# Performance work log

Measured on AMD Instinct MI355X. Metric: run time of the kernel, lower is better.

Reference implementation:

```python
import jax, jax.numpy as jnp
import numpy as np

B, N, D, H, DEPTH = 2, 2048, 768, 12, 4
DH = D // H
SCALE = DH ** -0.5
EPS = 1e-5
FF = 4 * D


def layer_norm(x, w, b):
    m = jnp.mean(x, axis=-1, keepdims=True)
    v = jnp.mean((x - m) ** 2, axis=-1, keepdims=True)
    return (x - m) * jax.lax.rsqrt(v + EPS) * w + b


def to_heads(t):  # [b, n, D] -> [b, H, n, DH]
    b, n, _ = t.shape
    return t.reshape(b, n, H, DH).transpose(0, 2, 1, 3)


def merge_heads(t):  # [b, H, n, DH] -> [b, n, D]
    b, h, n, dh = t.shape
    return t.transpose(0, 2, 1, 3).reshape(b, n, D)


def attend(q, k, v, bias):
    s = jnp.einsum('bhid,bhjd->bhij', q, k) * SCALE + bias
    a = jax.nn.softmax(s, axis=-1)
    return merge_heads(jnp.einsum('bhij,bhjd->bhid', a, v))


def setup_inputs():
    key = jax.random.key(0)
    ks = iter(jax.random.split(key, 16))

    def p(shape, scale=0.02):
        return jax.random.normal(next(ks), shape, dtype=jnp.float32) * scale

    inp = {
        'x': jax.random.normal(next(ks), (B, N, D), dtype=jnp.float32),
        'context': jax.random.normal(next(ks), (B, N, D), dtype=jnp.float32),
        'relative_position_bias': jax.random.normal(next(ks), (1, H, N, N), dtype=jnp.float32) * 0.02,
        # self-attn params (stacked over depth)
        'ln1_w': jnp.ones((DEPTH, D), jnp.float32), 'ln1_b': jnp.zeros((DEPTH, D), jnp.float32),
        'w_qkv': p((DEPTH, D, 3 * D)),
        'w_so': p((DEPTH, D, D)), 'b_so': jnp.zeros((DEPTH, D), jnp.float32),
        # cross-attn params (shared LN applied to x and context, as in source)
        'ln2_w': jnp.ones((DEPTH, D), jnp.float32), 'ln2_b': jnp.zeros((DEPTH, D), jnp.float32),
        'w_q': p((DEPTH, D, D)), 'w_k': p((DEPTH, D, D)), 'w_v': p((DEPTH, D, D)),
        'w_co': p((DEPTH, D, D)), 'b_co': jnp.zeros((DEPTH, D), jnp.float32),
        # FFN params
        'ln3_w': jnp.ones((DEPTH, D), jnp.float32), 'ln3_b': jnp.zeros((DEPTH, D), jnp.float32),
        'w_f1': p((DEPTH, D, FF)), 'b_f1': jnp.zeros((DEPTH, FF), jnp.float32),
        'w_f2': p((DEPTH, FF, D)), 'b_f2': jnp.zeros((DEPTH, D), jnp.float32),
        # final norm
        'lnout_w': jnp.ones((D,), jnp.float32), 'lnout_b': jnp.zeros((D,), jnp.float32),
    }
    return inp


def reference(x, context, relative_position_bias,
              ln1_w, ln1_b, w_qkv, w_so, b_so,
              ln2_w, ln2_b, w_q, w_k, w_v, w_co, b_co,
              ln3_w, ln3_b, w_f1, b_f1, w_f2, b_f2,
              lnout_w, lnout_b):
    bias = relative_position_bias
    for i in range(DEPTH):
        # self-attention block (pre-norm, residual)
        xn = layer_norm(x, ln1_w[i], ln1_b[i])
        q, k, v = jnp.split(xn @ w_qkv[i], 3, axis=-1)
        o = attend(to_heads(q), to_heads(k), to_heads(v), bias)
        x = o @ w_so[i] + b_so[i] + x
        # cross-attention block (input_norm shared for x and context)
        xn = layer_norm(x, ln2_w[i], ln2_b[i])
        cn = layer_norm(context, ln2_w[i], ln2_b[i])
        o = attend(to_heads(xn @ w_q[i]), to_heads(cn @ w_k[i]), to_heads(cn @ w_v[i]), bias)
        x = o @ w_co[i] + b_co[i] + x
        # FFN block
        xn = layer_norm(x, ln3_w[i], ln3_b[i])
        h = jax.nn.gelu(xn @ w_f1[i] + b_f1[i], approximate=False)
        x = h @ w_f2[i] + b_f2[i] + x
    return layer_norm(x, lnout_w, lnout_b)
```

## Files before the change

kernel.cpp:

```cpp
#include <hip/hip_runtime.h>
#include <cstdint>
#include <cstddef>

#define DEV static __device__ __forceinline__

typedef float  f32x4 __attribute__((ext_vector_type(4)));
typedef float  f32x2 __attribute__((ext_vector_type(2)));
typedef short  s16x8 __attribute__((ext_vector_type(8)));
typedef unsigned short u16;
typedef unsigned int   u32;
typedef unsigned int   u32x4 __attribute__((ext_vector_type(4)));
typedef unsigned short u16x2 __attribute__((ext_vector_type(2)));
typedef unsigned short u16x4 __attribute__((ext_vector_type(4)));
typedef __bf16 bf16x8 __attribute__((ext_vector_type(8)));

#define LOG2E 1.4426950408889634f
#define QSCALE_CONST 0.18033688011112042f
#define BSCALE 256.0f
#define BINV   0.00390625f

DEV u16 f2bf(float f){ return __builtin_bit_cast(u16, (__bf16)f); }
DEV float bf2f(u16 v){ union { unsigned u; float f; } x; x.u = ((unsigned)v) << 16; return x.f; }

DEV float fexp2(float x){
#if __has_builtin(__builtin_amdgcn_exp2f)
  return __builtin_amdgcn_exp2f(x);
#else
  return exp2f(x);
#endif
}

DEV f32x4 mfma16(s16x8 a, s16x8 b, f32x4 c){
  return __builtin_amdgcn_mfma_f32_16x16x32_bf16(
      __builtin_bit_cast(bf16x8, a), __builtin_bit_cast(bf16x8, b), c, 0, 0, 0);
}

DEV void gld16(const void* g, void* l){
  __builtin_amdgcn_global_load_lds(
      (const __attribute__((address_space(1))) void*)(uintptr_t)g,
      (__attribute__((address_space(3))) void*)(unsigned)(uintptr_t)l,
      16, 0, 0);
}

#if __has_builtin(__builtin_amdgcn_cvt_pk_fp8_f32) && __has_builtin(__builtin_amdgcn_cvt_pk_f32_fp8)
DEV u32 pk4_fp8(f32x4 v){
  int r = __builtin_amdgcn_cvt_pk_fp8_f32(v[0], v[1], 0, false);
  r     = __builtin_amdgcn_cvt_pk_fp8_f32(v[2], v[3], r, true);
  return (u32)r;
}
template<bool HI>
DEV f32x2 upk_fp8(u32 w){
  return __builtin_amdgcn_cvt_pk_f32_fp8((int)w, HI);
}
#else
DEV unsigned enc1(float x){
  union{float f; unsigned u;} c; c.f = x;
  unsigned s = (c.u >> 24) & 0x80;
  int e = (int)((c.u >> 23) & 0xff) - 127;
  unsigned m = c.u & 0x7fffff;
  if (e >= -6){
    unsigned mant = m >> 20, rem = m & 0xfffff;
    if (rem > 0x80000 || (rem == 0x80000 && (mant & 1))) mant++;
    unsigned eb = (unsigned)(e + 7);
    if (mant == 8){ mant = 0; eb++; }
    if (eb >= 16){ eb = 15; mant = 6; }
    return s | (eb << 3) | mant;
  }
  if (e < -10) return s;
  int sh = -6 - e;
  unsigned full = (1u << 23) | m;
  unsigned mant = full >> (20 + sh);
  unsigned rem  = full & ((1u << (20 + sh)) - 1);
  unsigned half = 1u << (19 + sh);
  if (rem > half || (rem == half && (mant & 1))) mant++;
  if (mant == 8) return s | (1u << 3);
  return s | mant;
}
DEV u32 pk4_fp8(f32x4 v){
  return enc1(v[0]) | (enc1(v[1]) << 8) | (enc1(v[2]) << 16) | (enc1(v[3]) << 24);
}
DEV float dec1(unsigned b){
  int s = (b >> 7) & 1, e = (b >> 3) & 15; float m = (float)(b & 7) * 0.125f;
  float v = e ? ldexpf(1.0f + m, e - 7) : ldexpf(m, -6);
  return s ? -v : v;
}
template<bool HI>
DEV f32x2 upk_fp8(u32 w){
  unsigned lo = HI ? ((w >> 16) & 0xff) : (w & 0xff);
  unsigned h2 = HI ? ((w >> 24) & 0xff) : ((w >> 8) & 0xff);
  f32x2 r; r[0] = dec1(lo); r[1] = dec1(h2); return r;
}
#endif

__global__ void __launch_bounds__(256)
transpose_cvt(const float* __restrict__ src, u16* __restrict__ dst, int K, int N,
              size_t dzstride){
  int z = blockIdx.z;
  src += (size_t)z * K * N;
  dst += (size_t)z * dzstride;
  __shared__ float t[32][33];
  int n0 = blockIdx.x * 32, k0 = blockIdx.y * 32;
#pragma unroll
  for (int i = 0; i < 4; ++i)
    t[threadIdx.y + 8*i][threadIdx.x] = src[(size_t)(k0 + threadIdx.y + 8*i) * N + n0 + threadIdx.x];
  __syncthreads();
#pragma unroll
  for (int i = 0; i < 4; ++i)
    dst[(size_t)(n0 + threadIdx.y + 8*i) * K + k0 + threadIdx.x] = f2bf(t[threadIdx.x][threadIdx.y + 8*i]);
}

struct TPtrs { const float* src[20]; u16* dst[20]; };
__global__ void __launch_bounds__(256)
transpose_cvt_batch(TPtrs tp){
  const float* src = tp.src[blockIdx.z];
  u16* dst = tp.dst[blockIdx.z];
  __shared__ float t[32][33];
  int n0 = blockIdx.x * 32, k0 = blockIdx.y * 32;
#pragma unroll
  for (int i = 0; i < 4; ++i)
    t[threadIdx.y + 8*i][threadIdx.x] = src[(size_t)(k0 + threadIdx.y + 8*i) * 768 + n0 + threadIdx.x];
  __syncthreads();
#pragma unroll
  for (int i = 0; i < 4; ++i)
    dst[(size_t)(n0 + threadIdx.y + 8*i) * 768 + k0 + threadIdx.x] = f2bf(t[threadIdx.x][threadIdx.y + 8*i]);
}

__global__ void __launch_bounds__(256)
cvt_biasT(const float* __restrict__ in, unsigned char* __restrict__ out){
  const int kvt = blockIdx.x, qt = blockIdx.y, h = blockIdx.z, tid = threadIdx.x;
  const int q  = qt * 64 + ((tid >> 6) << 4) + (tid & 15);
  const int c0 = kvt * 64 + ((tid >> 4) & 3) * 4;
  const float* src = in + ((size_t)h * 2048 + q) * 2048;
  u32x4 wv;
#pragma unroll
  for (int mi = 0; mi < 4; ++mi){
    f32x4 v = *(const f32x4*)(src + c0 + mi * 16);
#pragma unroll
    for (int r = 0; r < 4; ++r) v[r] = fminf(fmaxf(v[r] * (LOG2E * BSCALE), -448.f), 448.f);
    wv[mi] = pk4_fp8(v);
  }
  *(u32x4*)(out + ((size_t)(h * 32 + qt) * 32 + kvt) * 4096 + tid * 16) = wv;
}

__global__ void __launch_bounds__(256)
ln_pre(const float* __restrict__ x, const float* __restrict__ ctx,
       const float* __restrict__ w1, const float* __restrict__ b1,
       const float* __restrict__ w2, const float* __restrict__ b2,
       u16* __restrict__ xn, u16* __restrict__ xbuf, u16* __restrict__ cn){
  const int wv = threadIdx.x >> 6, lane = threadIdx.x & 63;
  const int row = blockIdx.x * 4 + wv;
  const float* xr = (blockIdx.y == 0 ? x : ctx) + (size_t)row * 768;
  f32x4 t[3]; float s = 0.f, s2 = 0.f;
#pragma unroll
  for (int c = 0; c < 3; ++c){
    t[c] = *(const f32x4*)(xr + c * 256 + lane * 4);
#pragma unroll
    for (int j = 0; j < 4; ++j){ s += t[c][j]; s2 += t[c][j] * t[c][j]; }
  }
#pragma unroll
  for (int off = 1; off < 64; off <<= 1){ s += __shfl_xor(s, off); s2 += __shfl_xor(s2, off); }
  float m = s * (1.f/768.f);
  float rstd = rsqrtf(s2 * (1.f/768.f) - m * m + 1e-5f);
  if (blockIdx.y == 0){
#pragma unroll
    for (int c = 0; c < 3; ++c){
      const int col = c * 256 + lane * 4;
      f32x4 wv4 = *(const f32x4*)(w1 + col);
      f32x4 bv4 = *(const f32x4*)(b1 + col);
      u16x4 o, xb;
#pragma unroll
      for (int j = 0; j < 4; ++j){
        o[j]  = f2bf((t[c][j] - m) * rstd * wv4[j] + bv4[j]);
        xb[j] = f2bf(t[c][j]);
      }
      *(u16x4*)(xn   + (size_t)row * 768 + col) = o;
      *(u16x4*)(xbuf + (size_t)row * 768 + col) = xb;
    }
  } else {
#pragma unroll
    for (int i = 0; i < 4; ++i){
      u16* dst = cn + (size_t)i * 4096 * 768 + (size_t)row * 768;
#pragma unroll
      for (int c = 0; c < 3; ++c){
        const int col = c * 256 + lane * 4;
        f32x4 wv4 = *(const f32x4*)(w2 + i * 768 + col);
        f32x4 bv4 = *(const f32x4*)(b2 + i * 768 + col);
        u16x4 o;
#pragma unroll
        for (int j = 0; j < 4; ++j) o[j] = f2bf((t[c][j] - m) * rstd * wv4[j] + bv4[j]);
        *(u16x4*)(dst + col) = o;
      }
    }
  }
}

template<typename OUT, int NZ>
__global__ void __launch_bounds__(256)
red_ln(const u16* __restrict__ pb, const float* __restrict__ biasrow,
       u16* __restrict__ xbuf, OUT* __restrict__ out,
       const float* __restrict__ lw, const float* __restrict__ lb){
  const int wv = threadIdx.x >> 6, lane = threadIdx.x & 63;
  const int row0 = blockIdx.x * 8 + wv * 2;
  const size_t S = 4096ll * 768;
  f32x4 t[2][3]; float s[2] = {0.f, 0.f}, s2[2] = {0.f, 0.f};
#pragma unroll
  for (int rr = 0; rr < 2; ++rr){
    const int row = row0 + rr;
    const u16* p0 = pb + (size_t)row * 768;
    u16* xr = xbuf + (size_t)row * 768;
#pragma unroll
    for (int c = 0; c < 3; ++c){
      const int col = c * 256 + lane * 4;
      f32x4 v = *(const f32x4*)(biasrow + col);
      u16x4 xv = *(const u16x4*)(xr + col);
#pragma unroll
      for (int j = 0; j < 4; ++j) v[j] += bf2f(xv[j]);
#pragma unroll
      for (int z = 0; z < NZ; ++z){
        u16x4 pv = *(const u16x4*)(p0 + z * S + col);
#pragma unroll
        for (int j = 0; j < 4; ++j) v[j] += bf2f(pv[j]);
      }
      u16x4 xo;
#pragma unroll
      for (int j = 0; j < 4; ++j) xo[j] = f2bf(v[j]);
      *(u16x4*)(xr + col) = xo;
      t[rr][c] = v;
#pragma unroll
      for (int j = 0; j < 4; ++j){ s[rr] += v[j]; s2[rr] += v[j] * v[j]; }
    }
  }
#pragma unroll
  for (int off = 1; off < 64; off <<= 1){
#pragma unroll
    for (int rr = 0; rr < 2; ++rr){
      s[rr]  += __shfl_xor(s[rr], off);
      s2[rr] += __shfl_xor(s2[rr], off);
    }
  }
#pragma unroll
  for (int rr = 0; rr < 2; ++rr){
    const int row = row0 + rr;
    float m = s[rr] * (1.f/768.f);
    float rstd = rsqrtf(s2[rr] * (1.f/768.f) - m * m + 1e-5f);
#pragma unroll
    for (int c = 0; c < 3; ++c){
      const int col = c * 256 + lane * 4;
      f32x4 wv4 = *(const f32x4*)(lw + col);
      f32x4 bv4 = *(const f32x4*)(lb + col);
      if constexpr (sizeof(OUT) == 2){
        u16x4 o;
#pragma unroll
        for (int j = 0; j < 4; ++j) o[j] = f2bf((t[rr][c][j] - m) * rstd * wv4[j] + bv4[j]);
        *(u16x4*)((u16*)out + (size_t)row * 768 + col) = o;
      } else {
        f32x4 o;
#pragma unroll
        for (int j = 0; j < 4; ++j) o[j] = (t[rr][c][j] - m) * rstd * wv4[j] + bv4[j];
        *(f32x4*)((float*)out + (size_t)row * 768 + col) = o;
      }
    }
  }
}

template<int EPI>
__global__ void __launch_bounds__(256)
gemm_bf16(const u16* __restrict__ A, int lda, const u16* __restrict__ Bt, int ldb,
          int nk, u16* __restrict__ Cb, int ldc,
          const float* __restrict__ bias,
          const u16* __restrict__ A2, const u16* __restrict__ Bt2){
  __shared__ u16 As[2][128 * 32];
  __shared__ u16 Bs[2][128 * 32];
  float colscale = 1.0f;
  if constexpr (EPI == 4){
    const int z = blockIdx.z;
    if (z == 0){ colscale = QSCALE_CONST; }
    else { A = A2; Bt = Bt2 + (size_t)(z - 1) * 768 * 768; }
    Cb += z * 768;
  }
  if constexpr (EPI == 5){
    const int z = blockIdx.z;
    A  += (size_t)z * nk * 32;
    Bt += (size_t)z * nk * 32;
    Cb += (size_t)z * 4096 * 768;
  }
  const int gx = gridDim.x, nwg = gx * gridDim.y;
  int lin = blockIdx.y * gx + blockIdx.x;
  {
    const int qq = nwg >> 3, rr = nwg & 7;
    const int xc = lin & 7, oo = lin >> 3;
    lin = (xc < rr ? xc * (qq + 1) : rr * (qq + 1) + (xc - rr) * qq) + oo;
  }
  const int m0 = (lin % gx) * 128, n0 = (lin / gx) * 128;

  const int tid = threadIdx.x, w = tid >> 6, lane = tid & 63;
  const int l16 = lane & 15, g = lane >> 4;
  const int wm = (w >> 1) * 64, wn = (w & 1) * 64;
  f32x4 acc[4][4] = {};

  const u16* a0 = A  + (size_t)(m0 + (tid >> 2)) * lda + (tid & 3) * 8;
  const u16* a1 = A  + (size_t)(m0 + (tid >> 2) + 64) * lda + (tid & 3) * 8;
  const u16* b0 = Bt + (size_t)(n0 + (tid >> 2)) * ldb + (tid & 3) * 8;
  const u16* b1 = Bt + (size_t)(n0 + (tid >> 2) + 64) * ldb + (tid & 3) * 8;

  {
    char* ab = (char*)As[0]; char* bb = (char*)Bs[0];
    gld16(a0, ab + w * 1024); gld16(a1, ab + 4096 + w * 1024);
    gld16(b0, bb + w * 1024); gld16(b1, bb + 4096 + w * 1024);
  }
  __syncthreads();

  int cb = 0;
  for (int kt = 0; kt < nk; ++kt){
    if (kt + 1 < nk){
      const int k1 = (kt + 1) * 32;
      char* ab = (char*)As[cb ^ 1]; char* bb = (char*)Bs[cb ^ 1];
      gld16(a0 + k1, ab + w * 1024); gld16(a1 + k1, ab + 4096 + w * 1024);
      gld16(b0 + k1, bb + w * 1024); gld16(b1 + k1, bb + 4096 + w * 1024);
    }
    const u16* Ab = As[cb]; const u16* Bb = Bs[cb];
    s16x8 af[4], bfv[4];
#pragma unroll
    for (int mi = 0; mi < 4; ++mi)
      af[mi] = *(const s16x8*)(Ab + (wm + mi*16 + l16) * 32 + 8 * g);
#pragma unroll
    for (int ni = 0; ni < 4; ++ni)
      bfv[ni] = *(const s16x8*)(Bb + (wn + ni*16 + l16) * 32 + 8 * g);
#pragma unroll
    for (int mi = 0; mi < 4; ++mi)
#pragma unroll
      for (int ni = 0; ni < 4; ++ni)
        acc[mi][ni] = mfma16(af[mi], bfv[ni], acc[mi][ni]);
    __syncthreads();
    cb ^= 1;
  }

#pragma unroll
  for (int mi = 0; mi < 4; ++mi){
    const int rg = m0 + wm + mi*16 + 4*g;
#pragma unroll
    for (int ni = 0; ni < 4; ++ni){
      const int col = n0 + wn + ni*16 + l16;
      f32x4 v = acc[mi][ni];
#pragma unroll
      for (int r = 0; r < 4; ++r){
        const int row = rg + r;
        if constexpr (EPI == 2){
          float t = v[r] + bias[col];
          float ge = 0.5f * t * (1.0f + erff(t * 0.7071067811865476f));
          Cb[(size_t)row * ldc + col] = f2bf(ge);
        } else if constexpr (EPI == 3){
          float sc = (col < 768) ? QSCALE_CONST : 1.0f;
          Cb[(size_t)row * ldc + col] = f2bf(v[r] * sc);
        } else if constexpr (EPI == 4){
          Cb[(size_t)row * ldc + col] = f2bf(v[r] * colscale);
        } else {
          Cb[(size_t)row * 768 + col] = f2bf(v[r]);
        }
      }
    }
  }
}

__global__ void __launch_bounds__(256)
attn_kernel(const u16* __restrict__ qkv, const unsigned char* __restrict__ biasT,
            u16* __restrict__ out){
  __shared__ __align__(16) u16 Ks[2][4096];
  __shared__ __align__(16) u16 Vt[2][4096];
  __shared__ __align__(16) u16 Pl[4][1024];

  const int tid = threadIdx.x, w = tid >> 6, lane = tid & 63;
  const int l16 = lane & 15, g = lane >> 4;
  const int qt = blockIdx.x, h = blockIdx.y, b = blockIdx.z;
  const int rowbase = b * 2048, q0 = qt * 64;

  const int ci0 = w * 64 + lane, ci1 = ci0 + 256;
  const int r0 = ci0 >> 3, sc0 = ci0 & 7, r1 = ci1 >> 3, sc1 = ci1 & 7;
  const u16* kp0 = qkv + (size_t)(rowbase + r0) * 2304 + 768 + h * 64 + (((sc0 ^ (r0 & 7)) & 7) << 3);
  const u16* kp1 = qkv + (size_t)(rowbase + r1) * 2304 + 768 + h * 64 + (((sc1 ^ (r1 & 7)) & 7) << 3);
  const int dh0 = (tid & 31) * 2, vs = tid >> 5;
  const u16* vp = qkv + (size_t)(rowbase + vs * 8) * 2304 + 1536 + h * 64 + dh0;
  u16x2 vr[8];
  const unsigned char* bT = biasT + ((size_t)(h * 32 + qt) * 32) * 4096 + tid * 16;
  u32x4 brW, bnW;

  const u16* qrow = qkv + (size_t)(rowbase + q0 + w * 16 + l16) * 2304 + h * 64;
  s16x8 qf0 = *(const s16x8*)(qrow + 8 * g);
  s16x8 qf1 = *(const s16x8*)(qrow + 32 + 8 * g);

  f32x4 oacc[4] = {};
  float mrun = -3.0e38f, lrun = 0.f;
  const int sw = l16 & 7;

  {
    char* kb = (char*)Ks[0] + w * 1024;
    gld16(kp0, kb); gld16(kp1, kb + 4096);
#pragma unroll
    for (int i = 0; i < 8; ++i) vr[i] = *(const u16x2*)(vp + (size_t)i * 2304);
    brW = *(const u32x4*)(bT);
    s16x8 vA, vB;
#pragma unroll
    for (int j = 0; j < 8; ++j){ vA[j] = (short)vr[j][0]; vB[j] = (short)vr[j][1]; }
    *(s16x8*)(Vt[0] + dh0 * 64 + ((vs ^ (dh0 & 7)) << 3)) = vA;
    *(s16x8*)(Vt[0] + (dh0 + 1) * 64 + ((vs ^ ((dh0 + 1) & 7)) << 3)) = vB;
  }
  __syncthreads();

  for (int t = 0; t < 32; ++t){
    const int cb = t & 1;
    if (t < 31){
      const size_t koff = (size_t)(t + 1) * 64 * 2304;
      char* kb = (char*)Ks[cb ^ 1] + w * 1024;
      gld16(kp0 + koff, kb); gld16(kp1 + koff, kb + 4096);
      const u16* p = vp + koff;
#pragma unroll
      for (int i = 0; i < 8; ++i) vr[i] = *(const u16x2*)(p + (size_t)i * 2304);
      bnW = *(const u32x4*)(bT + (size_t)(t + 1) * 4096);
    }

    f32x4 st[4];
    __builtin_amdgcn_s_setprio(1);
#pragma unroll
    for (int mi = 0; mi < 4; ++mi){
      const int row = l16 + 16 * mi;
      s16x8 kf0 = *(const s16x8*)(Ks[cb] + row * 64 + ((g ^ sw) << 3));
      s16x8 kf1 = *(const s16x8*)(Ks[cb] + row * 64 + (((g + 4) ^ sw) << 3));
      f32x4 z = {};
      z = mfma16(kf0, qf0, z);
      st[mi] = mfma16(kf1, qf1, z);
    }
    __builtin_amdgcn_s_setprio(0);

    float mloc[4];
#pragma unroll
    for (int mi = 0; mi < 4; ++mi){
      f32x2 lo = upk_fp8<false>(brW[mi]);
      f32x2 hi = upk_fp8<true>(brW[mi]);
      st[mi][0] = fmaf(lo[0], BINV, st[mi][0]);
      st[mi][1] = fmaf(lo[1], BINV, st[mi][1]);
      st[mi][2] = fmaf(hi[0], BINV, st[mi][2]);
      st[mi][3] = fmaf(hi[1], BINV, st[mi][3]);
      mloc[mi] = fmaxf(fmaxf(st[mi][0], st[mi][1]), fmaxf(st[mi][2], st[mi][3]));
    }
    float tmax = fmaxf(fmaxf(mloc[0], mloc[1]), fmaxf(mloc[2], mloc[3]));
    tmax = fmaxf(tmax, __shfl_xor(tmax, 16));
    tmax = fmaxf(tmax, __shfl_xor(tmax, 32));
    if (!__all(tmax <= mrun + 8.f)){
      float mnew = fmaxf(mrun, tmax);
      float al = fexp2(mrun - mnew);
      mrun = mnew;
      lrun *= al;
#pragma unroll
      for (int r = 0; r < 4; ++r){
        float aq = __shfl(al, 4 * g + r);
#pragma unroll
        for (int ni = 0; ni < 4; ++ni) oacc[ni][r] *= aq;
      }
    }
    float ssum = 0.f;
#pragma unroll
    for (int mi = 0; mi < 4; ++mi){
      u16x4 pk;
#pragma unroll
      for (int r = 0; r < 4; ++r){
        float pv = fexp2(st[mi][r] - mrun);
        ssum += pv;
        pk[r] = f2bf(pv);
      }
      *(u16x4*)(Pl[w] + l16 * 64 + (((2*mi + (g >> 1)) ^ sw) << 3) + 4 * (g & 1)) = pk;
    }
    ssum += __shfl_xor(ssum, 16);
    ssum += __shfl_xor(ssum, 32);
    lrun += ssum;

    __builtin_amdgcn_s_setprio(1);
#pragma unroll
    for (int ks2 = 0; ks2 < 2; ++ks2){
      s16x8 pf = *(const s16x8*)(Pl[w] + l16 * 64 + (((4*ks2 + g) ^ sw) << 3));
#pragma unroll
      for (int ni = 0; ni < 4; ++ni){
        const int dh = l16 + 16 * ni;
        s16x8 vf = *(const s16x8*)(Vt[cb] + dh * 64 + (((4*ks2 + g) ^ sw) << 3));
        oacc[ni] = mfma16(pf, vf, oacc[ni]);
      }
    }
    __builtin_amdgcn_s_setprio(0);

    if (t < 31){
      s16x8 vA, vB;
#pragma unroll
      for (int j = 0; j < 8; ++j){ vA[j] = (short)vr[j][0]; vB[j] = (short)vr[j][1]; }
      *(s16x8*)(Vt[cb ^ 1] + dh0 * 64 + ((vs ^ (dh0 & 7)) << 3)) = vA;
      *(s16x8*)(Vt[cb ^ 1] + (dh0 + 1) * 64 + ((vs ^ ((dh0 + 1) & 7)) << 3)) = vB;
      brW = bnW;
    }
    __syncthreads();
  }

#pragma unroll
  for (int r = 0; r < 4; ++r){
    float lq = __shfl(lrun, 4 * g + r);
    float inv = 1.0f / lq;
    const int row = rowbase + q0 + w * 16 + 4 * g + r;
#pragma unroll
    for (int ni = 0; ni < 4; ++ni)
      out[(size_t)row * 768 + h * 64 + l16 + 16 * ni] = f2bf(oacc[ni][r] * inv);
  }
}

extern "C" void kernel_launch(void* const* d_in, const int* in_sizes, int n_in,
                              void* d_out, int out_size, void* d_ws, size_t ws_size,
                              hipStream_t stream){
  const float* in_x    = (const float*)d_in[0];
  const float* in_ctx  = (const float*)d_in[1];
  const float* in_bias = (const float*)d_in[2];
  const float* ln1_w = (const float*)d_in[3];
  const float* ln1_b = (const float*)d_in[4];
  const float* w_qkv = (const float*)d_in[5];
  const float* w_so  = (const float*)d_in[6];
  const float* b_so  = (const float*)d_in[7];
  const float* ln2_w = (const float*)d_in[8];
  const float* ln2_b = (const float*)d_in[9];
  const float* w_q   = (const float*)d_in[10];
  const float* w_k   = (const float*)d_in[11];
  const float* w_v   = (const float*)d_in[12];
  const float* w_co  = (const float*)d_in[13];
  const float* b_co  = (const float*)d_in[14];
  const float* ln3_w = (const float*)d_in[15];
  const float* ln3_b = (const float*)d_in[16];
  const float* w_f1  = (const float*)d_in[17];
  const float* b_f1  = (const float*)d_in[18];
  const float* w_f2  = (const float*)d_in[19];
  const float* b_f2  = (const float*)d_in[20];
  const float* lnout_w = (const float*)d_in[21];
  const float* lnout_b = (const float*)d_in[22];

  char* p = (char*)d_ws;
  u16* xbuf    = (u16*)p;    p += 4096ll * 768 * 2;
  u16* pbuf    = (u16*)p;    p += 4ll * 4096 * 768 * 2;
  u16* xn      = (u16*)p;    p += 4096ll * 768 * 2;
  u16* cn      = (u16*)p;    p += 4ll * 4096 * 768 * 2;
  u16* qkvb    = (u16*)p;    p += 4096ll * 2304 * 2;
  u16* attO    = (u16*)p;    p += 4096ll * 768 * 2;
  u16* ffh     = (u16*)p;    p += 4096ll * 3072 * 2;
  u16* wqkvT   = (u16*)p;    p += 4ll * 2304 * 768 * 2;
  u16* wsoT    = (u16*)p;    p += 4ll * 768 * 768 * 2;
  u16* wqT     = (u16*)p;    p += 4ll * 768 * 768 * 2;
  u16* wkvT    = (u16*)p;    p += 4ll * 1536 * 768 * 2;
  u16* wcoT    = (u16*)p;    p += 4ll * 768 * 768 * 2;
  u16* wf1T    = (u16*)p;    p += 4ll * 3072 * 768 * 2;
  u16* wf2T    = (u16*)p;    p += 4ll * 768 * 3072 * 2;
  unsigned char* biasT = (unsigned char*)p; p += 12ll * 2048 * 2048;

  const dim3 tb(32, 8);
  transpose_cvt<<<dim3(72, 24, 4), tb, 0, stream>>>(w_qkv, wqkvT, 768, 2304, 2304ll*768);
  transpose_cvt<<<dim3(96, 24, 4), tb, 0, stream>>>(w_f1,  wf1T,  768, 3072, 3072ll*768);
  transpose_cvt<<<dim3(24, 96, 4), tb, 0, stream>>>(w_f2,  wf2T,  3072, 768, 768ll*3072);
  {
    TPtrs tp;
    for (int i = 0; i < 4; ++i){
      tp.src[i*5+0] = w_so + (size_t)i*768*768;  tp.dst[i*5+0] = wsoT + (size_t)i*768*768;
      tp.src[i*5+1] = w_q  + (size_t)i*768*768;  tp.dst[i*5+1] = wqT  + (size_t)i*768*768;
      tp.src[i*5+2] = w_k  + (size_t)i*768*768;  tp.dst[i*5+2] = wkvT + (size_t)i*1536*768;
      tp.src[i*5+3] = w_v  + (size_t)i*768*768;  tp.dst[i*5+3] = wkvT + (size_t)i*1536*768 + 768ll*768;
      tp.src[i*5+4] = w_co + (size_t)i*768*768;  tp.dst[i*5+4] = wcoT + (size_t)i*768*768;
    }
    transpose_cvt_batch<<<dim3(24, 24, 20), tb, 0, stream>>>(tp);
  }
  cvt_biasT<<<dim3(32, 32, 12), 256, 0, stream>>>(in_bias, biasT);
  ln_pre<<<dim3(1024, 2), 256, 0, stream>>>(in_x, in_ctx, ln1_w, ln1_b, ln2_w, ln2_b,
                                            xn, xbuf, cn);

  const dim3 ag(32, 12, 2);
  for (int i = 0; i < 4; ++i){
    gemm_bf16<3><<<dim3(32, 18), 256, 0, stream>>>(xn, 768, wqkvT + (size_t)i*2304*768, 768, 24,
                                                   qkvb, 2304, nullptr, nullptr, nullptr);
    attn_kernel<<<ag, 256, 0, stream>>>(qkvb, biasT, attO);
    gemm_bf16<5><<<dim3(32, 6, 2), 256, 0, stream>>>(attO, 768, wsoT + (size_t)i*768*768, 768, 12,
                                                     pbuf, 768, nullptr, nullptr, nullptr);
    red_ln<u16,2><<<512, 256, 0, stream>>>(pbuf, b_so + i*768, xbuf, xn, ln2_w + i*768, ln2_b + i*768);
    gemm_bf16<4><<<dim3(32, 6, 3), 256, 0, stream>>>(xn, 768, wqT + (size_t)i*768*768, 768, 24,
                                                     qkvb, 2304, nullptr,
                                                     cn + (size_t)i*4096*768, wkvT + (size_t)i*1536*768);
    attn_kernel<<<ag, 256, 0, stream>>>(qkvb, biasT, attO);
    gemm_bf16<5><<<dim3(32, 6, 2), 256, 0, stream>>>(attO, 768, wcoT + (size_t)i*768*768, 768, 12,
                                                     pbuf, 768, nullptr, nullptr, nullptr);
    red_ln<u16,2><<<512, 256, 0, stream>>>(pbuf, b_co + i*768, xbuf, xn, ln3_w + i*768, ln3_b + i*768);
    gemm_bf16<2><<<dim3(32, 24), 256, 0, stream>>>(xn, 768, wf1T + (size_t)i*3072*768, 768, 24,
                                                   ffh, 3072, b_f1 + i*3072, nullptr, nullptr);
    gemm_bf16<5><<<dim3(32, 6, 4), 256, 0, stream>>>(ffh, 3072, wf2T + (size_t)i*768*3072, 3072, 24,
                                                     pbuf, 768, nullptr, nullptr, nullptr);
    if (i < 3)
      red_ln<u16,4><<<512, 256, 0, stream>>>(pbuf, b_f2 + i*768, xbuf, xn, ln1_w + (i+1)*768, ln1_b + (i+1)*768);
    else
      red_ln<float,4><<<512, 256, 0, stream>>>(pbuf, b_f2 + i*768, xbuf, (float*)d_out, lnout_w, lnout_b);
  }
}
```

Measured before the change: 1.273 ms.

## Use 2 waves per attention block, each handling 32 query rows

The attention kernel now runs 128 threads (2 waves) per 64-query tile instead of 4 waves, with each wave processing two 16-row query groups. Every K/V fragment read from LDS feeds two MFMAs, which reduces LDS traffic per FLOP and halves the number of threads issuing global loads per block. The cost is higher per-thread register use (double accumulators, 16 V regs) and fewer waves available to hide latency.

```diff
diff --git a/kernel.cpp b/kernel.cpp
--- a/kernel.cpp
+++ b/kernel.cpp
@@ -362,47 +362,64 @@
   }
 }
 
-__global__ void __launch_bounds__(256)
+__global__ void __launch_bounds__(128)
 attn_kernel(const u16* __restrict__ qkv, const unsigned char* __restrict__ biasT,
             u16* __restrict__ out){
   __shared__ __align__(16) u16 Ks[2][4096];
   __shared__ __align__(16) u16 Vt[2][4096];
-  __shared__ __align__(16) u16 Pl[4][1024];
+  __shared__ __align__(16) u16 Pl[2][2048];
 
   const int tid = threadIdx.x, w = tid >> 6, lane = tid & 63;
   const int l16 = lane & 15, g = lane >> 4;
   const int qt = blockIdx.x, h = blockIdx.y, b = blockIdx.z;
   const int rowbase = b * 2048, q0 = qt * 64;
 
-  const int ci0 = w * 64 + lane, ci1 = ci0 + 256;
-  const int r0 = ci0 >> 3, sc0 = ci0 & 7, r1 = ci1 >> 3, sc1 = ci1 & 7;
-  const u16* kp0 = qkv + (size_t)(rowbase + r0) * 2304 + 768 + h * 64 + (((sc0 ^ (r0 & 7)) & 7) << 3);
-  const u16* kp1 = qkv + (size_t)(rowbase + r1) * 2304 + 768 + h * 64 + (((sc1 ^ (r1 & 7)) & 7) << 3);
+  const u16* kp[4];
+#pragma unroll
+  for (int i = 0; i < 4; ++i){
+    const int ci = tid + 128 * i;
+    const int r = ci >> 3, sc = ci & 7;
+    kp[i] = qkv + (size_t)(rowbase + r) * 2304 + 768 + h * 64 + (((sc ^ (r & 7)) & 7) << 3);
+  }
   const int dh0 = (tid & 31) * 2, vs = tid >> 5;
-  const u16* vp = qkv + (size_t)(rowbase + vs * 8) * 2304 + 1536 + h * 64 + dh0;
-  u16x2 vr[8];
-  const unsigned char* bT = biasT + ((size_t)(h * 32 + qt) * 32) * 4096 + tid * 16;
-  u32x4 brW, bnW;
-
-  const u16* qrow = qkv + (size_t)(rowbase + q0 + w * 16 + l16) * 2304 + h * 64;
-  s16x8 qf0 = *(const s16x8*)(qrow + 8 * g);
-  s16x8 qf1 = *(const s16x8*)(qrow + 32 + 8 * g);
-
-  f32x4 oacc[4] = {};
-  float mrun = -3.0e38f, lrun = 0.f;
+  const u16* vp = qkv + (size_t)(rowbase + vs * 16) * 2304 + 1536 + h * 64 + dh0;
+  u16x2 vr[16];
+  const unsigned char* bTbase = biasT + ((size_t)(h * 32 + qt) * 32) * 4096;
+  const unsigned char* bTn[2] = {
+    bTbase + (size_t)(((2 * w + 0) << 6) | (g << 4) | l16) * 16,
+    bTbase + (size_t)(((2 * w + 1) << 6) | (g << 4) | l16) * 16 };
+  u32x4 brW[2], bnW[2];
+
+  s16x8 qf0[2], qf1[2];
+#pragma unroll
+  for (int ni = 0; ni < 2; ++ni){
+    const u16* qrow = qkv + (size_t)(rowbase + q0 + w * 32 + 16 * ni + l16) * 2304 + h * 64;
+    qf0[ni] = *(const s16x8*)(qrow + 8 * g);
+    qf1[ni] = *(const s16x8*)(qrow + 32 + 8 * g);
+  }
+
+  f32x4 oacc[2][4] = {};
+  float mrun[2] = {-3.0e38f, -3.0e38f}, lrun[2] = {0.f, 0.f};
   const int sw = l16 & 7;
 
   {
-    char* kb = (char*)Ks[0] + w * 1024;
-    gld16(kp0, kb); gld16(kp1, kb + 4096);
-#pragma unroll
-    for (int i = 0; i < 8; ++i) vr[i] = *(const u16x2*)(vp + (size_t)i * 2304);
-    brW = *(const u32x4*)(bT);
-    s16x8 vA, vB;
-#pragma unroll
-    for (int j = 0; j < 8; ++j){ vA[j] = (short)vr[j][0]; vB[j] = (short)vr[j][1]; }
-    *(s16x8*)(Vt[0] + dh0 * 64 + ((vs ^ (dh0 & 7)) << 3)) = vA;
-    *(s16x8*)(Vt[0] + (dh0 + 1) * 64 + ((vs ^ ((dh0 + 1) & 7)) << 3)) = vB;
+#pragma unroll
+    for (int i = 0; i < 4; ++i)
+      gld16(kp[i], (char*)Ks[0] + w * 1024 + i * 2048);
+#pragma unroll
+    for (int i = 0; i < 16; ++i) vr[i] = *(const u16x2*)(vp + (size_t)i * 2304);
+    brW[0] = *(const u32x4*)(bTn[0]);
+    brW[1] = *(const u32x4*)(bTn[1]);
+    s16x8 vA0, vA1, vB0, vB1;
+#pragma unroll
+    for (int j = 0; j < 8; ++j){
+      vA0[j] = (short)vr[j][0];     vB0[j] = (short)vr[j][1];
+      vA1[j] = (short)vr[8 + j][0]; vB1[j] = (short)vr[8 + j][1];
+    }
+    *(s16x8*)(Vt[0] + dh0 * 64 + (((2 * vs    ) ^ (dh0 & 7)) << 3)) = vA0;
+    *(s16x8*)(Vt[0] + dh0 * 64 + (((2 * vs + 1) ^ (dh0 & 7)) << 3)) = vA1;
+    *(s16x8*)(Vt[0] + (dh0 + 1) * 64 + (((2 * vs    ) ^ ((dh0 + 1) & 7)) << 3)) = vB0;
+    *(s16x8*)(Vt[0] + (dh0 + 1) * 64 + (((2 * vs + 1) ^ ((dh0 + 1) & 7)) << 3)) = vB1;
   }
   __syncthreads();
 
@@ -410,101 +427,123 @@
     const int cb = t & 1;
     if (t < 31){
       const size_t koff = (size_t)(t + 1) * 64 * 2304;
-      char* kb = (char*)Ks[cb ^ 1] + w * 1024;
-      gld16(kp0 + koff, kb); gld16(kp1 + koff, kb + 4096);
+#pragma unroll
+      for (int i = 0; i < 4; ++i)
+        gld16(kp[i] + koff, (char*)Ks[cb ^ 1] + w * 1024 + i * 2048);
       const u16* p = vp + koff;
 #pragma unroll
-      for (int i = 0; i < 8; ++i) vr[i] = *(const u16x2*)(p + (size_t)i * 2304);
-      bnW = *(const u32x4*)(bT + (size_t)(t + 1) * 4096);
-    }
-
-    f32x4 st[4];
+      for (int i = 0; i < 16; ++i) vr[i] = *(const u16x2*)(p + (size_t)i * 2304);
+      bnW[0] = *(const u32x4*)(bTn[0] + (size_t)(t + 1) * 4096);
+      bnW[1] = *(const u32x4*)(bTn[1] + (size_t)(t + 1) * 4096);
+    }
+
+    f32x4 st[4][2];
     __builtin_amdgcn_s_setprio(1);
 #pragma unroll
     for (int mi = 0; mi < 4; ++mi){
       const int row = l16 + 16 * mi;
       s16x8 kf0 = *(const s16x8*)(Ks[cb] + row * 64 + ((g ^ sw) << 3));
       s16x8 kf1 = *(const s16x8*)(Ks[cb] + row * 64 + (((g + 4) ^ sw) << 3));
-      f32x4 z = {};
-      z = mfma16(kf0, qf0, z);
-      st[mi] = mfma16(kf1, qf1, z);
+#pragma unroll
+      for (int ni = 0; ni < 2; ++ni){
+        f32x4 z = {};
+        z = mfma16(kf0, qf0[ni], z);
+        st[mi][ni] = mfma16(kf1, qf1[ni], z);
+      }
     }
     __builtin_amdgcn_s_setprio(0);
 
-    float mloc[4];
-#pragma unroll
-    for (int mi = 0; mi < 4; ++mi){
-      f32x2 lo = upk_fp8<false>(brW[mi]);
-      f32x2 hi = upk_fp8<true>(brW[mi]);
-      st[mi][0] = fmaf(lo[0], BINV, st[mi][0]);
-      st[mi][1] = fmaf(lo[1], BINV, st[mi][1]);
-      st[mi][2] = fmaf(hi[0], BINV, st[mi][2]);
-      st[mi][3] = fmaf(hi[1], BINV, st[mi][3]);
-      mloc[mi] = fmaxf(fmaxf(st[mi][0], st[mi][1]), fmaxf(st[mi][2], st[mi][3]));
-    }
-    float tmax = fmaxf(fmaxf(mloc[0], mloc[1]), fmaxf(mloc[2], mloc[3]));
-    tmax = fmaxf(tmax, __shfl_xor(tmax, 16));
-    tmax = fmaxf(tmax, __shfl_xor(tmax, 32));
-    if (!__all(tmax <= mrun + 8.f)){
-      float mnew = fmaxf(mrun, tmax);
-      float al = fexp2(mrun - mnew);
-      mrun = mnew;
-      lrun *= al;
-#pragma unroll
-      for (int r = 0; r < 4; ++r){
-        float aq = __shfl(al, 4 * g + r);
-#pragma unroll
-        for (int ni = 0; ni < 4; ++ni) oacc[ni][r] *= aq;
-      }
-    }
-    float ssum = 0.f;
-#pragma unroll
-    for (int mi = 0; mi < 4; ++mi){
-      u16x4 pk;
-#pragma unroll
-      for (int r = 0; r < 4; ++r){
-        float pv = fexp2(st[mi][r] - mrun);
-        ssum += pv;
-        pk[r] = f2bf(pv);
-      }
-      *(u16x4*)(Pl[w] + l16 * 64 + (((2*mi + (g >> 1)) ^ sw) << 3) + 4 * (g & 1)) = pk;
-    }
-    ssum += __shfl_xor(ssum, 16);
-    ssum += __shfl_xor(ssum, 32);
-    lrun += ssum;
+#pragma unroll
+    for (int ni = 0; ni < 2; ++ni){
+      float mloc[4];
+#pragma unroll
+      for (int mi = 0; mi < 4; ++mi){
+        f32x2 lo = upk_fp8<false>(brW[ni][mi]);
+        f32x2 hi = upk_fp8<true>(brW[ni][mi]);
+        st[mi][ni][0] = fmaf(lo[0], BINV, st[mi][ni][0]);
+        st[mi][ni][1] = fmaf(lo[1], BINV, st[mi][ni][1]);
+        st[mi][ni][2] = fmaf(hi[0], BINV, st[mi][ni][2]);
+        st[mi][ni][3] = fmaf(hi[1], BINV, st[mi][ni][3]);
+        mloc[mi] = fmaxf(fmaxf(st[mi][ni][0], st[mi][ni][1]),
+                         fmaxf(st[mi][ni][2], st[mi][ni][3]));
+      }
+      float tmax = fmaxf(fmaxf(mloc[0], mloc[1]), fmaxf(mloc[2], mloc[3]));
+      tmax = fmaxf(tmax, __shfl_xor(tmax, 16));
+      tmax = fmaxf(tmax, __shfl_xor(tmax, 32));
+      if (!__all(tmax <= mrun[ni] + 8.f)){
+        float mnew = fmaxf(mrun[ni], tmax);
+        float al = fexp2(mrun[ni] - mnew);
+        mrun[ni] = mnew;
+        lrun[ni] *= al;
+#pragma unroll
+        for (int r = 0; r < 4; ++r){
+          float aq = __shfl(al, 4 * g + r);
+#pragma unroll
+          for (int ni2 = 0; ni2 < 4; ++ni2) oacc[ni][ni2][r] *= aq;
+        }
+      }
+      float ssum = 0.f;
+#pragma unroll
+      for (int mi = 0; mi < 4; ++mi){
+        u16x4 pk;
+#pragma unroll
+        for (int r = 0; r < 4; ++r){
+          float pv = fexp2(st[mi][ni][r] - mrun[ni]);
+          ssum += pv;
+          pk[r] = f2bf(pv);
+        }
+        *(u16x4*)(Pl[w] + (16 * ni + l16) * 64 + (((2*mi + (g >> 1)) ^ sw) << 3) + 4 * (g & 1)) = pk;
+      }
+      ssum += __shfl_xor(ssum, 16);
+      ssum += __shfl_xor(ssum, 32);
+      lrun[ni] += ssum;
+    }
 
     __builtin_amdgcn_s_setprio(1);
 #pragma unroll
     for (int ks2 = 0; ks2 < 2; ++ks2){
-      s16x8 pf = *(const s16x8*)(Pl[w] + l16 * 64 + (((4*ks2 + g) ^ sw) << 3));
-#pragma unroll
-      for (int ni = 0; ni < 4; ++ni){
-        const int dh = l16 + 16 * ni;
+      s16x8 pf[2];
+#pragma unroll
+      for (int ni = 0; ni < 2; ++ni)
+        pf[ni] = *(const s16x8*)(Pl[w] + (16 * ni + l16) * 64 + (((4*ks2 + g) ^ sw) << 3));
+#pragma unroll
+      for (int ni2 = 0; ni2 < 4; ++ni2){
+        const int dh = l16 + 16 * ni2;
         s16x8 vf = *(const s16x8*)(Vt[cb] + dh * 64 + (((4*ks2 + g) ^ sw) << 3));
-        oacc[ni] = mfma16(pf, vf, oacc[ni]);
+#pragma unroll
+        for (int ni = 0; ni < 2; ++ni)
+          oacc[ni][ni2] = mfma16(pf[ni], vf, oacc[ni][ni2]);
       }
     }
     __builtin_amdgcn_s_setprio(0);
 
     if (t < 31){
-      s16x8 vA, vB;
-#pragma unroll
-      for (int j = 0; j < 8; ++j){ vA[j] = (short)vr[j][0]; vB[j] = (short)vr[j][1]; }
-      *(s16x8*)(Vt[cb ^ 1] + dh0 * 64 + ((vs ^ (dh0 & 7)) << 3)) = vA;
-      *(s16x8*)(Vt[cb ^ 1] + (dh0 + 1) * 64 + ((vs ^ ((dh0 + 1) & 7)) << 3)) = vB;
-      brW = bnW;
+      s16x8 vA0, vA1, vB0, vB1;
+#pragma unroll
+      for (int j = 0; j < 8; ++j){
+        vA0[j] = (short)vr[j][0];     vB0[j] = (short)vr[j][1];
+        vA1[j] = (short)vr[8 + j][0]; vB1[j] = (short)vr[8 + j][1];
+      }
+      *(s16x8*)(Vt[cb ^ 1] + dh0 * 64 + (((2 * vs    ) ^ (dh0 & 7)) << 3)) = vA0;
+      *(s16x8*)(Vt[cb ^ 1] + dh0 * 64 + (((2 * vs + 1) ^ (dh0 & 7)) << 3)) = vA1;
+      *(s16x8*)(Vt[cb ^ 1] + (dh0 + 1) * 64 + (((2 * vs    ) ^ ((dh0 + 1) & 7)) << 3)) = vB0;
+      *(s16x8*)(Vt[cb ^ 1] + (dh0 + 1) * 64 + (((2 * vs + 1) ^ ((dh0 + 1) & 7)) << 3)) = vB1;
+      brW[0] = bnW[0]; brW[1] = bnW[1];
     }
     __syncthreads();
   }
 
 #pragma unroll
-  for (int r = 0; r < 4; ++r){
-    float lq = __shfl(lrun, 4 * g + r);
-    float inv = 1.0f / lq;
-    const int row = rowbase + q0 + w * 16 + 4 * g + r;
-#pragma unroll
-    for (int ni = 0; ni < 4; ++ni)
-      out[(size_t)row * 768 + h * 64 + l16 + 16 * ni] = f2bf(oacc[ni][r] * inv);
+  for (int ni = 0; ni < 2; ++ni){
+#pragma unroll
+    for (int r = 0; r < 4; ++r){
+      float lq = __shfl(lrun[ni], 4 * g + r);
+      float inv = 1.0f / lq;
+      const int row = rowbase + q0 + w * 32 + 16 * ni + 4 * g + r;
+#pragma unroll
+      for (int ni2 = 0; ni2 < 4; ++ni2)
+        out[(size_t)row * 768 + h * 64 + l16 + 16 * ni2] = f2bf(oacc[ni][ni2][r] * inv);
+    }
   }
 }
 
@@ -575,14 +614,14 @@
   for (int i = 0; i < 4; ++i){
     gemm_bf16<3><<<dim3(32, 18), 256, 0, stream>>>(xn, 768, wqkvT + (size_t)i*2304*768, 768, 24,
                                                    qkvb, 2304, nullptr, nullptr, nullptr);
-    attn_kernel<<<ag, 256, 0, stream>>>(qkvb, biasT, attO);
+    attn_kernel<<<ag, 128, 0, stream>>>(qkvb, biasT, attO);
     gemm_bf16<5><<<dim3(32, 6, 2), 256, 0, stream>>>(attO, 768, wsoT + (size_t)i*768*768, 768, 12,
                                                      pbuf, 768, nullptr, nullptr, nullptr);
     red_ln<u16,2><<<512, 256, 0, stream>>>(pbuf, b_so + i*768, xbuf, xn, ln2_w + i*768, ln2_b + i*768);
     gemm_bf16<4><<<dim3(32, 6, 3), 256, 0, stream>>>(xn, 768, wqT + (size_t)i*768*768, 768, 24,
                                                      qkvb, 2304, nullptr,
                                                      cn + (size_t)i*4096*768, wkvT + (size_t)i*1536*768);
-    attn_kernel<<<ag, 256, 0, stream>>>(qkvb, biasT, attO);
+    attn_kernel<<<ag, 128, 0, stream>>>(qkvb, biasT, attO);
     gemm_bf16<5><<<dim3(32, 6, 2), 256, 0, stream>>>(attO, 768, wcoT + (size_t)i*768*768, 768, 12,
                                                      pbuf, 768, nullptr, nullptr, nullptr);
     red_ln<u16,2><<<512, 256, 0, stream>>>(pbuf, b_co + i*768, xbuf, xn, ln3_w + i*768, ln3_b + i*768);
```

New measurement: 1.374 ms. 1.08x slower.
